# Performance work log

Hardware: AMD Instinct MI355X
Metric: run time of the kernel (lower is better)

## Reference

```python
import jax, jax.numpy as jnp
import numpy as np

N, E = 50000, 400000
IN_DIM, OUT_DIM, EDGE_DIM, HEADS = 128, 32, 64, 8
N_REL = 512
NEG_SLOPE = 0.2  # GATv2 leaky_relu slope


def setup_inputs() -> dict:
    key = jax.random.key(0)
    ks = jax.random.split(key, 12)
    HC = HEADS * OUT_DIM
    return {
        "x": jax.random.normal(ks[0], (N, IN_DIM), jnp.float32),
        "edge_index": jax.random.randint(ks[1], (2, E), 0, N),
        "relations": jax.random.normal(ks[2], (N_REL, EDGE_DIM), jnp.float32),
        "relation_index": jax.random.randint(ks[3], (E,), 0, N_REL),
        "W_l": jax.random.normal(ks[4], (IN_DIM, HC), jnp.float32) / np.sqrt(IN_DIM),
        "b_l": jnp.zeros((HC,), jnp.float32),
        "W_r": jax.random.normal(ks[5], (IN_DIM, HC), jnp.float32) / np.sqrt(IN_DIM),
        "b_r": jnp.zeros((HC,), jnp.float32),
        "W_e": jax.random.normal(ks[6], (EDGE_DIM, HC), jnp.float32) / np.sqrt(EDGE_DIM),
        "att": jax.random.normal(ks[7], (HEADS, OUT_DIM), jnp.float32) / np.sqrt(OUT_DIM),
        "bias": jnp.zeros((OUT_DIM,), jnp.float32),
    }


def reference(x, edge_index, relations, relation_index, W_l, b_l, W_r, b_r, W_e, att, bias):
    H, C = HEADS, OUT_DIM
    src, dst = edge_index[0], edge_index[1]
    edge_attr = relations[relation_index]                       # [E, edge_dim]

    # add_self_loops with fill_value='mean': self-loop attr = mean of incoming edge_attr
    deg = jax.ops.segment_sum(jnp.ones((E,), x.dtype), dst, num_segments=N)
    attr_sum = jax.ops.segment_sum(edge_attr, dst, num_segments=N)
    self_attr = attr_sum / jnp.maximum(deg, 1.0)[:, None]        # [N, edge_dim]

    loop = jnp.arange(N)
    src_f = jnp.concatenate([src, loop])                         # [E+N]
    dst_f = jnp.concatenate([dst, loop])
    ea_f = jnp.concatenate([edge_attr, self_attr], axis=0)       # [E+N, edge_dim]

    x_l = (x @ W_l + b_l).reshape(N, H, C)
    x_r = (x @ W_r + b_r).reshape(N, H, C)
    e_emb = (ea_f @ W_e).reshape(-1, H, C)                       # [E+N, H, C]

    # GATv2 scoring: leaky_relu(x_l[src] + x_r[dst] + e_emb) . att
    m = x_l[src_f] + x_r[dst_f] + e_emb                          # [E+N, H, C]
    m = jnp.where(m >= 0, m, NEG_SLOPE * m)
    logits = jnp.einsum("ehc,hc->eh", m, att)                    # [E+N, H]

    # segment softmax over destination node
    lmax = jax.ops.segment_max(logits, dst_f, num_segments=N)    # [N, H]
    ex = jnp.exp(logits - lmax[dst_f])
    denom = jax.ops.segment_sum(ex, dst_f, num_segments=N)       # [N, H]
    alpha = ex / denom[dst_f]                                    # [E+N, H]

    # scatter-add aggregation of alpha-weighted source features
    msg = alpha[:, :, None] * x_l[src_f]                         # [E+N, H, C]
    out = jax.ops.segment_sum(msg, dst_f, num_segments=N)        # [N, H, C]
    out = out.mean(axis=1) + bias                                # concat=False -> head mean
    return (out, relations)
```

## Files before the change

### kernel.cpp

```cpp
#include <hip/hip_runtime.h>

#define N_NODES   50000
#define N_EDGES   400000
#define IN_DIM    128
#define OUT_DIM   32
#define EDGE_DIM  64
#define HEADS     8
#define HC        256
#define N_REL     512
#define NEG_SLOPE 0.2f
#define NB_SCAN   196

__global__ void k_rel_emb(const float* __restrict__ relations,
                          const float* __restrict__ W_e,
                          float* __restrict__ rel_emb) {
    __shared__ float row[EDGE_DIM];
    const int r = blockIdx.x;
    const int j = threadIdx.x;
    if (j < EDGE_DIM) row[j] = relations[r * EDGE_DIM + j];
    __syncthreads();
    float acc = 0.f;
#pragma unroll
    for (int k = 0; k < EDGE_DIM; ++k)
        acc = fmaf(row[k], W_e[k * HC + j], acc);
    rel_emb[r * HC + j] = acc;
}

__global__ void k_deg(const int* __restrict__ dst_arr, int* __restrict__ deg_i) {
    const int e = blockIdx.x * 256 + threadIdx.x;
    if (e < N_EDGES) atomicAdd(&deg_i[dst_arr[e]], 1);
}

__global__ void __launch_bounds__(256) k_scan_a(const int* __restrict__ deg_i,
                                                int* __restrict__ incl,
                                                int* __restrict__ partials) {
    __shared__ int s[256];
    const int i = blockIdx.x * 256 + threadIdx.x;
    const int v = (i < N_NODES) ? deg_i[i] : 0;
    s[threadIdx.x] = v;
    __syncthreads();
#pragma unroll
    for (int o = 1; o < 256; o <<= 1) {
        int t = s[threadIdx.x];
        if (threadIdx.x >= o) t += s[threadIdx.x - o];
        __syncthreads();
        s[threadIdx.x] = t;
        __syncthreads();
    }
    if (i < N_NODES) incl[i] = s[threadIdx.x];
    if (threadIdx.x == 255) partials[blockIdx.x] = s[255];
}

__global__ void __launch_bounds__(256) k_scan_b(int* __restrict__ partials) {
    __shared__ int s[256];
    const int v = (threadIdx.x < NB_SCAN) ? partials[threadIdx.x] : 0;
    s[threadIdx.x] = v;
    __syncthreads();
#pragma unroll
    for (int o = 1; o < 256; o <<= 1) {
        int t = s[threadIdx.x];
        if (threadIdx.x >= o) t += s[threadIdx.x - o];
        __syncthreads();
        s[threadIdx.x] = t;
        __syncthreads();
    }
    if (threadIdx.x < NB_SCAN) partials[threadIdx.x] = s[threadIdx.x] - v;
}

__global__ void __launch_bounds__(256) k_scan_c(const int* __restrict__ incl,
                                                const int* __restrict__ deg_i,
                                                const int* __restrict__ partials,
                                                int* __restrict__ row_ptr) {
    const int i = blockIdx.x * 256 + threadIdx.x;
    if (i < N_NODES) row_ptr[i] = incl[i] - deg_i[i] + partials[blockIdx.x];
    if (i == 0) row_ptr[N_NODES] = N_EDGES;
}

__global__ void k_fill(const int* __restrict__ src_arr,
                       const int* __restrict__ dst_arr,
                       const int* __restrict__ rel_idx,
                       const int* __restrict__ row_ptr,
                       int* __restrict__ cursor,
                       int2* __restrict__ csr) {
    const int e = blockIdx.x * 256 + threadIdx.x;
    if (e >= N_EDGES) return;
    const int d = dst_arr[e];
    const int pos = row_ptr[d] + atomicAdd(&cursor[d], 1);
    csr[pos] = make_int2(src_arr[e], rel_idx[e]);
}

__global__ void __launch_bounds__(256) k_selfattr(
        const int* __restrict__ row_ptr, const int2* __restrict__ csr,
        const float* __restrict__ relations, float* __restrict__ self_attr) {
    const int n = (blockIdx.x * 256 + threadIdx.x) >> 6;
    if (n >= N_NODES) return;
    const int lane = threadIdx.x & 63;
    const int beg = row_ptr[n], end = row_ptr[n + 1];
    float a = 0.f;
    for (int i = beg; i < end; ++i) {
        const int r = csr[i].y;
        a += relations[r * EDGE_DIM + lane];
    }
    const float dg = (float)max(end - beg, 1);
    self_attr[n * EDGE_DIM + lane] = a / dg;
}

__global__ void __launch_bounds__(256) k_node(
        const float* __restrict__ x,
        const float* __restrict__ W_l, const float* __restrict__ b_l,
        const float* __restrict__ W_r, const float* __restrict__ b_r,
        const float* __restrict__ W_e,
        const float* __restrict__ self_attr,
        float* __restrict__ x_l, float* __restrict__ x_r,
        float* __restrict__ self_emb) {
    __shared__ float xs[8][IN_DIM];
    __shared__ float as[8][EDGE_DIM];
    const int n0 = blockIdx.x * 8;
    const int j = threadIdx.x;
    for (int t = j; t < 8 * IN_DIM; t += 256) {
        const int ni = t >> 7, k = t & 127;
        xs[ni][k] = x[(size_t)(n0 + ni) * IN_DIM + k];
    }
    for (int t = j; t < 8 * EDGE_DIM; t += 256) {
        const int ni = t >> 6, k = t & 63;
        as[ni][k] = self_attr[(size_t)(n0 + ni) * EDGE_DIM + k];
    }
    __syncthreads();
    const float bl = b_l[j], br = b_r[j];
    float al[8], ar[8], ae[8];
#pragma unroll
    for (int ni = 0; ni < 8; ++ni) { al[ni] = bl; ar[ni] = br; ae[ni] = 0.f; }

    for (int k = 0; k < IN_DIM; k += 4) {
        const float wl0 = W_l[(k + 0) * HC + j], wl1 = W_l[(k + 1) * HC + j];
        const float wl2 = W_l[(k + 2) * HC + j], wl3 = W_l[(k + 3) * HC + j];
        const float wr0 = W_r[(k + 0) * HC + j], wr1 = W_r[(k + 1) * HC + j];
        const float wr2 = W_r[(k + 2) * HC + j], wr3 = W_r[(k + 3) * HC + j];
#pragma unroll
        for (int ni = 0; ni < 8; ++ni) {
            const float4 xv = *(const float4*)&xs[ni][k];
            al[ni] = fmaf(xv.x, wl0, fmaf(xv.y, wl1, fmaf(xv.z, wl2, fmaf(xv.w, wl3, al[ni]))));
            ar[ni] = fmaf(xv.x, wr0, fmaf(xv.y, wr1, fmaf(xv.z, wr2, fmaf(xv.w, wr3, ar[ni]))));
        }
    }
    for (int k = 0; k < EDGE_DIM; k += 4) {
        const float we0 = W_e[(k + 0) * HC + j], we1 = W_e[(k + 1) * HC + j];
        const float we2 = W_e[(k + 2) * HC + j], we3 = W_e[(k + 3) * HC + j];
#pragma unroll
        for (int ni = 0; ni < 8; ++ni) {
            const float4 av = *(const float4*)&as[ni][k];
            ae[ni] = fmaf(av.x, we0, fmaf(av.y, we1, fmaf(av.z, we2, fmaf(av.w, we3, ae[ni]))));
        }
    }
#pragma unroll
    for (int ni = 0; ni < 8; ++ni) {
        x_l[(size_t)(n0 + ni) * HC + j] = al[ni];
        x_r[(size_t)(n0 + ni) * HC + j] = ar[ni];
        self_emb[(size_t)(n0 + ni) * HC + j] = ae[ni];
    }
}

__global__ void __launch_bounds__(256) k_agg(
        const int* __restrict__ row_ptr, const int2* __restrict__ csr,
        const float* __restrict__ x_l, const float* __restrict__ x_r,
        const float* __restrict__ rel_emb, const float* __restrict__ self_emb,
        const float* __restrict__ att, const float* __restrict__ bias,
        float* __restrict__ out) {
    const int n = (blockIdx.x * 256 + threadIdx.x) >> 6;
    if (n >= N_NODES) return;
    const int lane = threadIdx.x & 63;
    const int q = lane & 7;
    const int off = (lane >> 3) * OUT_DIM + q * 4;

    const float4 at = *(const float4*)(att + off);
    const float4 xr = *(const float4*)(x_r + (size_t)n * HC + off);

    const float4 xls = *(const float4*)(x_l + (size_t)n * HC + off);
    const float4 se  = *(const float4*)(self_emb + (size_t)n * HC + off);
    float m0 = xls.x + xr.x + se.x; m0 = m0 >= 0.f ? m0 : NEG_SLOPE * m0;
    float m1 = xls.y + xr.y + se.y; m1 = m1 >= 0.f ? m1 : NEG_SLOPE * m1;
    float m2 = xls.z + xr.z + se.z; m2 = m2 >= 0.f ? m2 : NEG_SLOPE * m2;
    float m3 = xls.w + xr.w + se.w; m3 = m3 >= 0.f ? m3 : NEG_SLOPE * m3;
    float p = at.x * m0 + at.y * m1 + at.z * m2 + at.w * m3;
    p += __shfl_xor(p, 1);
    p += __shfl_xor(p, 2);
    p += __shfl_xor(p, 4);
    float ex = __expf(p);
    float den = ex;
    float4 acc;
    acc.x = ex * xls.x; acc.y = ex * xls.y; acc.z = ex * xls.z; acc.w = ex * xls.w;

    const int beg = row_ptr[n], end = row_ptr[n + 1];
    for (int i = beg; i < end; ++i) {
        const int2 sr = csr[i];
        const float4 xl = *(const float4*)(x_l + (size_t)sr.x * HC + off);
        const float4 ev = *(const float4*)(rel_emb + (size_t)sr.y * HC + off);
        float a0 = xl.x + xr.x + ev.x; a0 = a0 >= 0.f ? a0 : NEG_SLOPE * a0;
        float a1 = xl.y + xr.y + ev.y; a1 = a1 >= 0.f ? a1 : NEG_SLOPE * a1;
        float a2 = xl.z + xr.z + ev.z; a2 = a2 >= 0.f ? a2 : NEG_SLOPE * a2;
        float a3 = xl.w + xr.w + ev.w; a3 = a3 >= 0.f ? a3 : NEG_SLOPE * a3;
        float pp = at.x * a0 + at.y * a1 + at.z * a2 + at.w * a3;
        pp += __shfl_xor(pp, 1);
        pp += __shfl_xor(pp, 2);
        pp += __shfl_xor(pp, 4);
        const float e2 = __expf(pp);
        den += e2;
        acc.x = fmaf(e2, xl.x, acc.x);
        acc.y = fmaf(e2, xl.y, acc.y);
        acc.z = fmaf(e2, xl.z, acc.z);
        acc.w = fmaf(e2, xl.w, acc.w);
    }

    const float inv = 1.f / den;
    float4 v;
    v.x = acc.x * inv; v.y = acc.y * inv; v.z = acc.z * inv; v.w = acc.w * inv;
    v.x += __shfl_xor(v.x, 8);  v.y += __shfl_xor(v.y, 8);
    v.z += __shfl_xor(v.z, 8);  v.w += __shfl_xor(v.w, 8);
    v.x += __shfl_xor(v.x, 16); v.y += __shfl_xor(v.y, 16);
    v.z += __shfl_xor(v.z, 16); v.w += __shfl_xor(v.w, 16);
    v.x += __shfl_xor(v.x, 32); v.y += __shfl_xor(v.y, 32);
    v.z += __shfl_xor(v.z, 32); v.w += __shfl_xor(v.w, 32);
    if (lane < 8) {
        const float4 bs = *(const float4*)(bias + q * 4);
        float4 o;
        o.x = v.x * 0.125f + bs.x;
        o.y = v.y * 0.125f + bs.y;
        o.z = v.z * 0.125f + bs.z;
        o.w = v.w * 0.125f + bs.w;
        *(float4*)(out + (size_t)n * OUT_DIM + q * 4) = o;
    }
}

__global__ void k_copy_rel(const float* __restrict__ relations,
                           float* __restrict__ out_tail) {
    const int i = blockIdx.x * 256 + threadIdx.x;
    if (i < N_REL * EDGE_DIM) out_tail[i] = relations[i];
}

extern "C" void kernel_launch(void* const* d_in, const int* in_sizes, int n_in,
                              void* d_out, int out_size, void* d_ws, size_t ws_size,
                              hipStream_t stream) {
    const float* x         = (const float*)d_in[0];
    const int*   edge_idx  = (const int*)d_in[1];
    const float* relations = (const float*)d_in[2];
    const int*   rel_idx   = (const int*)d_in[3];
    const float* W_l       = (const float*)d_in[4];
    const float* b_l       = (const float*)d_in[5];
    const float* W_r       = (const float*)d_in[6];
    const float* b_r       = (const float*)d_in[7];
    const float* W_e       = (const float*)d_in[8];
    const float* att       = (const float*)d_in[9];
    const float* bias      = (const float*)d_in[10];

    const int* src_arr = edge_idx;
    const int* dst_arr = edge_idx + N_EDGES;

    float* out      = (float*)d_out;
    float* out_tail = out + N_NODES * OUT_DIM;

    float* ws        = (float*)d_ws;
    float* x_l       = ws;
    float* x_r       = x_l + (size_t)N_NODES * HC;
    float* self_emb  = x_r + (size_t)N_NODES * HC;
    float* rel_emb   = self_emb + (size_t)N_NODES * HC;
    float* self_attr = rel_emb + (size_t)N_REL * HC;
    int*   ibase     = (int*)(self_attr + (size_t)N_NODES * EDGE_DIM);
    int2*  csr       = (int2*)ibase;
    int*   row_ptr   = ibase + 2 * N_EDGES;
    int*   incl      = row_ptr + N_NODES + 4;
    int*   deg_i     = incl + N_NODES;
    int*   cursor    = deg_i + N_NODES;
    int*   partials  = cursor + N_NODES;

    hipMemsetAsync(deg_i, 0, 2 * N_NODES * sizeof(int), stream);

    k_rel_emb<<<N_REL, 256, 0, stream>>>(relations, W_e, rel_emb);

    k_deg<<<(N_EDGES + 255) / 256, 256, 0, stream>>>(dst_arr, deg_i);
    k_scan_a<<<NB_SCAN, 256, 0, stream>>>(deg_i, incl, partials);
    k_scan_b<<<1, 256, 0, stream>>>(partials);
    k_scan_c<<<NB_SCAN, 256, 0, stream>>>(incl, deg_i, partials, row_ptr);
    k_fill<<<(N_EDGES + 255) / 256, 256, 0, stream>>>(
        src_arr, dst_arr, rel_idx, row_ptr, cursor, csr);

    k_selfattr<<<(N_NODES * 64 + 255) / 256, 256, 0, stream>>>(
        row_ptr, csr, relations, self_attr);

    k_node<<<N_NODES / 8, 256, 0, stream>>>(
        x, W_l, b_l, W_r, b_r, W_e, self_attr, x_l, x_r, self_emb);

    k_agg<<<(N_NODES * 64 + 255) / 256, 256, 0, stream>>>(
        row_ptr, csr, x_l, x_r, rel_emb, self_emb, att, bias, out);

    k_final_unused:;
    k_copy_rel<<<(N_REL * EDGE_DIM + 255) / 256, 256, 0, stream>>>(
        relations, out_tail);
}
```

Measured before the change: 389.3 us.

## Replace per-node projection kernel with register-tiled shared-memory GEMM kernels

Replaces the fused per-node projection kernel (8 nodes per block, weights read from global per thread) and the relation-embedding kernel with a generic 64x64 tiled GEMM that stages A and W tiles in shared memory and computes a 4x4 register tile per thread. The goal is to raise arithmetic intensity and cut redundant global weight loads for the x@W_l, x@W_r, self_attr@W_e and relations@W_e products. In exchange, x is read twice and there are four launches instead of one fused kernel.

```diff
diff --git a/kernel.cpp b/kernel.cpp
--- a/kernel.cpp
+++ b/kernel.cpp
@@ -10,20 +10,90 @@
 #define N_REL     512
 #define NEG_SLOPE 0.2f
 #define NB_SCAN   196
-
-__global__ void k_rel_emb(const float* __restrict__ relations,
-                          const float* __restrict__ W_e,
-                          float* __restrict__ rel_emb) {
-    __shared__ float row[EDGE_DIM];
-    const int r = blockIdx.x;
-    const int j = threadIdx.x;
-    if (j < EDGE_DIM) row[j] = relations[r * EDGE_DIM + j];
-    __syncthreads();
-    float acc = 0.f;
-#pragma unroll
-    for (int k = 0; k < EDGE_DIM; ++k)
-        acc = fmaf(row[k], W_e[k * HC + j], acc);
-    rel_emb[r * HC + j] = acc;
+#define KT        64
+
+template<int K>
+__global__ __launch_bounds__(256) void k_gemm(
+        const float* __restrict__ A, const float* __restrict__ W,
+        const float* __restrict__ bias, float* __restrict__ C, int M) {
+    __shared__ float As[64][KT + 4];
+    __shared__ float Ws[KT][64];
+    const int bid = blockIdx.x;
+    const int mt = bid >> 2, ct = bid & 3;
+    const int n0 = mt * 64;
+    const int c0 = ct * 64;
+    const int t  = threadIdx.x;
+    const int tx = t & 15, ty = t >> 4;
+
+    float acc[4][4];
+    if (bias) {
+        const float4 b4 = *(const float4*)(bias + c0 + tx * 4);
+#pragma unroll
+        for (int mi = 0; mi < 4; ++mi) {
+            acc[mi][0] = b4.x; acc[mi][1] = b4.y;
+            acc[mi][2] = b4.z; acc[mi][3] = b4.w;
+        }
+    } else {
+#pragma unroll
+        for (int mi = 0; mi < 4; ++mi)
+#pragma unroll
+            for (int ci = 0; ci < 4; ++ci) acc[mi][ci] = 0.f;
+    }
+
+    for (int kt = 0; kt < K; kt += KT) {
+#pragma unroll
+        for (int i = t * 4; i < 64 * KT; i += 1024) {
+            const int node = i >> 6;
+            const int kk   = i & 63;
+            const int row  = n0 + node;
+            float4 v = make_float4(0.f, 0.f, 0.f, 0.f);
+            if (row < M) v = *(const float4*)(A + (size_t)row * K + kt + kk);
+            *(float4*)&As[node][kk] = v;
+        }
+#pragma unroll
+        for (int i = t * 4; i < KT * 64; i += 1024) {
+            const int kk = i >> 6;
+            const int c  = i & 63;
+            *(float4*)&Ws[kk][c] =
+                *(const float4*)(W + (size_t)(kt + kk) * HC + c0 + c);
+        }
+        __syncthreads();
+
+#pragma unroll
+        for (int k = 0; k < KT; k += 4) {
+            const float4 a0 = *(const float4*)&As[ty * 4 + 0][k];
+            const float4 a1 = *(const float4*)&As[ty * 4 + 1][k];
+            const float4 a2 = *(const float4*)&As[ty * 4 + 2][k];
+            const float4 a3 = *(const float4*)&As[ty * 4 + 3][k];
+            const float4 w0 = *(const float4*)&Ws[k + 0][tx * 4];
+            const float4 w1 = *(const float4*)&Ws[k + 1][tx * 4];
+            const float4 w2 = *(const float4*)&Ws[k + 2][tx * 4];
+            const float4 w3 = *(const float4*)&Ws[k + 3][tx * 4];
+#define GSTEP(mi, AV)                                                          \
+            acc[mi][0] = fmaf(AV.x, w0.x, fmaf(AV.y, w1.x,                     \
+                         fmaf(AV.z, w2.x, fmaf(AV.w, w3.x, acc[mi][0]))));     \
+            acc[mi][1] = fmaf(AV.x, w0.y, fmaf(AV.y, w1.y,                     \
+                         fmaf(AV.z, w2.y, fmaf(AV.w, w3.y, acc[mi][1]))));     \
+            acc[mi][2] = fmaf(AV.x, w0.z, fmaf(AV.y, w1.z,                     \
+                         fmaf(AV.z, w2.z, fmaf(AV.w, w3.z, acc[mi][2]))));     \
+            acc[mi][3] = fmaf(AV.x, w0.w, fmaf(AV.y, w1.w,                     \
+                         fmaf(AV.z, w2.w, fmaf(AV.w, w3.w, acc[mi][3]))))
+            GSTEP(0, a0); GSTEP(1, a1); GSTEP(2, a2); GSTEP(3, a3);
+#undef GSTEP
+        }
+        __syncthreads();
+    }
+
+#pragma unroll
+    for (int mi = 0; mi < 4; ++mi) {
+        const int row = n0 + ty * 4 + mi;
+        if (row < M) {
+            float4 o;
+            o.x = acc[mi][0]; o.y = acc[mi][1];
+            o.z = acc[mi][2]; o.w = acc[mi][3];
+            *(float4*)(C + (size_t)row * HC + c0 + tx * 4) = o;
+        }
+    }
 }
 
 __global__ void k_deg(const int* __restrict__ dst_arr, int* __restrict__ deg_i) {
@@ -103,61 +173,6 @@
     }
     const float dg = (float)max(end - beg, 1);
     self_attr[n * EDGE_DIM + lane] = a / dg;
-}
-
-__global__ void __launch_bounds__(256) k_node(
-        const float* __restrict__ x,
-        const float* __restrict__ W_l, const float* __restrict__ b_l,
-        const float* __restrict__ W_r, const float* __restrict__ b_r,
-        const float* __restrict__ W_e,
-        const float* __restrict__ self_attr,
-        float* __restrict__ x_l, float* __restrict__ x_r,
-        float* __restrict__ self_emb) {
-    __shared__ float xs[8][IN_DIM];
-    __shared__ float as[8][EDGE_DIM];
-    const int n0 = blockIdx.x * 8;
-    const int j = threadIdx.x;
-    for (int t = j; t < 8 * IN_DIM; t += 256) {
-        const int ni = t >> 7, k = t & 127;
-        xs[ni][k] = x[(size_t)(n0 + ni) * IN_DIM + k];
-    }
-    for (int t = j; t < 8 * EDGE_DIM; t += 256) {
-        const int ni = t >> 6, k = t & 63;
-        as[ni][k] = self_attr[(size_t)(n0 + ni) * EDGE_DIM + k];
-    }
-    __syncthreads();
-    const float bl = b_l[j], br = b_r[j];
-    float al[8], ar[8], ae[8];
-#pragma unroll
-    for (int ni = 0; ni < 8; ++ni) { al[ni] = bl; ar[ni] = br; ae[ni] = 0.f; }
-
-    for (int k = 0; k < IN_DIM; k += 4) {
-        const float wl0 = W_l[(k + 0) * HC + j], wl1 = W_l[(k + 1) * HC + j];
-        const float wl2 = W_l[(k + 2) * HC + j], wl3 = W_l[(k + 3) * HC + j];
-        const float wr0 = W_r[(k + 0) * HC + j], wr1 = W_r[(k + 1) * HC + j];
-        const float wr2 = W_r[(k + 2) * HC + j], wr3 = W_r[(k + 3) * HC + j];
-#pragma unroll
-        for (int ni = 0; ni < 8; ++ni) {
-            const float4 xv = *(const float4*)&xs[ni][k];
-            al[ni] = fmaf(xv.x, wl0, fmaf(xv.y, wl1, fmaf(xv.z, wl2, fmaf(xv.w, wl3, al[ni]))));
-            ar[ni] = fmaf(xv.x, wr0, fmaf(xv.y, wr1, fmaf(xv.z, wr2, fmaf(xv.w, wr3, ar[ni]))));
-        }
-    }
-    for (int k = 0; k < EDGE_DIM; k += 4) {
-        const float we0 = W_e[(k + 0) * HC + j], we1 = W_e[(k + 1) * HC + j];
-        const float we2 = W_e[(k + 2) * HC + j], we3 = W_e[(k + 3) * HC + j];
-#pragma unroll
-        for (int ni = 0; ni < 8; ++ni) {
-            const float4 av = *(const float4*)&as[ni][k];
-            ae[ni] = fmaf(av.x, we0, fmaf(av.y, we1, fmaf(av.z, we2, fmaf(av.w, we3, ae[ni]))));
-        }
-    }
-#pragma unroll
-    for (int ni = 0; ni < 8; ++ni) {
-        x_l[(size_t)(n0 + ni) * HC + j] = al[ni];
-        x_r[(size_t)(n0 + ni) * HC + j] = ar[ni];
-        self_emb[(size_t)(n0 + ni) * HC + j] = ae[ni];
-    }
 }
 
 __global__ void __launch_bounds__(256) k_agg(
@@ -274,8 +289,6 @@
 
     hipMemsetAsync(deg_i, 0, 2 * N_NODES * sizeof(int), stream);
 
-    k_rel_emb<<<N_REL, 256, 0, stream>>>(relations, W_e, rel_emb);
-
     k_deg<<<(N_EDGES + 255) / 256, 256, 0, stream>>>(dst_arr, deg_i);
     k_scan_a<<<NB_SCAN, 256, 0, stream>>>(deg_i, incl, partials);
     k_scan_b<<<1, 256, 0, stream>>>(partials);
@@ -283,16 +296,21 @@
     k_fill<<<(N_EDGES + 255) / 256, 256, 0, stream>>>(
         src_arr, dst_arr, rel_idx, row_ptr, cursor, csr);
 
+    const int mt_nodes = (N_NODES + 63) / 64;
+    const int mt_rel   = (N_REL + 63) / 64;
+    k_gemm<128><<<mt_nodes * 4, 256, 0, stream>>>(x, W_l, b_l, x_l, N_NODES);
+    k_gemm<128><<<mt_nodes * 4, 256, 0, stream>>>(x, W_r, b_r, x_r, N_NODES);
+    k_gemm<64><<<mt_rel * 4, 256, 0, stream>>>(relations, W_e, nullptr,
+                                               rel_emb, N_REL);
+
     k_selfattr<<<(N_NODES * 64 + 255) / 256, 256, 0, stream>>>(
         row_ptr, csr, relations, self_attr);
-
-    k_node<<<N_NODES / 8, 256, 0, stream>>>(
-        x, W_l, b_l, W_r, b_r, W_e, self_attr, x_l, x_r, self_emb);
+    k_gemm<64><<<mt_nodes * 4, 256, 0, stream>>>(self_attr, W_e, nullptr,
+                                                 self_emb, N_NODES);
 
     k_agg<<<(N_NODES * 64 + 255) / 256, 256, 0, stream>>>(
         row_ptr, csr, x_l, x_r, rel_emb, self_emb, att, bias, out);
 
-    k_final_unused:;
     k_copy_rel<<<(N_REL * EDGE_DIM + 255) / 256, 256, 0, stream>>>(
         relations, out_tail);
 }
```

New measurement: 448.8 us. 15.3% more time.
